# Kernel optimization log

Measured on AMD Instinct MI355X. Metric: run time of the kernel, lower is better.

## Reference

```python
import jax, jax.numpy as jnp
import numpy as np

N = 100000      # nodes
E = 1600000     # directed edges (before self loops)
F_IN = 128      # n_features
H = 100         # hidden width of every GCNConv / fc1
N_HIDDEN = 8    # conv2..conv9


def setup_inputs() -> dict:
    key = jax.random.key(0)
    ks = jax.random.split(key, 12)
    s = 0.05
    x = jax.random.normal(ks[0], (N, F_IN), jnp.float32)
    edge_index = jax.random.randint(ks[1], (2, E), 0, N, dtype=jnp.int64)
    labels = (jax.random.uniform(ks[2], (N, 1)) < 0.1).astype(jnp.float32)
    W1 = jax.random.normal(ks[3], (F_IN, H), jnp.float32) * s
    b1 = jnp.zeros((H,), jnp.float32)
    Wh = jax.random.normal(ks[4], (N_HIDDEN, H, H), jnp.float32) * s
    bh = jnp.zeros((N_HIDDEN, H), jnp.float32)
    fc1_W = jax.random.normal(ks[5], (H, H), jnp.float32) * s
    fc1_b = jnp.zeros((H,), jnp.float32)
    fc2_W = jax.random.normal(ks[6], (H, 1), jnp.float32) * s
    fc2_b = jnp.zeros((1,), jnp.float32)
    return {"x": x, "edge_index": edge_index, "labels": labels,
            "W1": W1, "b1": b1, "Wh": Wh, "bh": bh,
            "fc1_W": fc1_W, "fc1_b": fc1_b, "fc2_W": fc2_W, "fc2_b": fc2_b}


def _gcn_conv(h, W, b, src, dst, norm):
    # linear transform, then degree-normalized scatter aggregation (PyG GCNConv)
    h = h @ W                                   # [N, H]
    msg = h[src] * norm[:, None]                # [E2, H] gather + scale
    agg = jax.ops.segment_sum(msg, dst, num_segments=N)  # scatter-add to [N, H]
    return agg + b


def reference(x, edge_index, labels, W1, b1, Wh, bh, fc1_W, fc1_b, fc2_W, fc2_b):
    # GCN normalization with self loops: norm_e = deg^-1/2[src] * deg^-1/2[dst]
    loops = jnp.arange(N, dtype=edge_index.dtype)
    src = jnp.concatenate([edge_index[0], loops])
    dst = jnp.concatenate([edge_index[1], loops])
    deg = jax.ops.segment_sum(jnp.ones_like(dst, jnp.float32), dst, num_segments=N)
    dinv = jax.lax.rsqrt(deg)                   # deg >= 1 due to self loops
    norm = dinv[src] * dinv[dst]

    # NOTE: source uses x.relu() (out-of-place, discarded) -> no nonlinearity;
    # dropout is identity in eval mode. Faithful reproduction below.
    h = _gcn_conv(x, W1, b1, src, dst, norm)
    for i in range(N_HIDDEN):
        h = _gcn_conv(h, Wh[i], bh[i], src, dst, norm)

    h = h @ fc1_W + fc1_b
    logits = h @ fc2_W + fc2_b
    p = jax.nn.sigmoid(logits)                  # [N, 1]

    # generate_weights: upweight positives by neg/pos ratio
    pos = labels.sum()
    w = ((jnp.float32(N) - pos) / pos) * labels + 1.0

    pc = jnp.clip(p, 1e-7, 1.0 - 1e-7)
    bce = -(labels * jnp.log(pc) + (1.0 - labels) * jnp.log(1.0 - pc))
    loss = jnp.mean(w * bce)
    return loss, p
```

## Files before the change

### kernel.cpp

```cpp
#include <hip/hip_runtime.h>
#include <hip/hip_fp16.h>
#include <math.h>

#define HW 100
#define FIN 128
#define NBLK 256
#define TPB 1024
#define CHUNK 392
#define PBLK 512
#define BCAP 64
#define ELDS 7424
#define M17 0x1FFFFu
#define NPADH 100352

typedef int iv4 __attribute__((ext_vector_type(4)));

__device__ __forceinline__ float ld_dev(const float* p) {
    return __hip_atomic_load(p, __ATOMIC_RELAXED, __HIP_MEMORY_SCOPE_AGENT);
}
__device__ __forceinline__ unsigned ld_devu(const unsigned* p) {
    return __hip_atomic_load(p, __ATOMIC_RELAXED, __HIP_MEMORY_SCOPE_AGENT);
}
__device__ __forceinline__ void st_devu(unsigned* p, unsigned v) {
    __hip_atomic_store(p, v, __ATOMIC_RELAXED, __HIP_MEMORY_SCOPE_AGENT);
}
__device__ __forceinline__ void st_devh(__half* p, __half v) {
    __hip_atomic_store(reinterpret_cast<unsigned short*>(p),
                       *reinterpret_cast<unsigned short*>(&v),
                       __ATOMIC_RELAXED, __HIP_MEMORY_SCOPE_AGENT);
}

__global__ __launch_bounds__(256) void k_prep(const int* __restrict__ src,
                                              const int* __restrict__ dst, int E4,
                                              unsigned* __restrict__ buckets,
                                              int* __restrict__ cnt,
                                              float* __restrict__ accums,
                                              unsigned* __restrict__ posDone,
                                              unsigned* __restrict__ fin,
                                              unsigned* __restrict__ flags,
                                              const float* __restrict__ W1, const float* __restrict__ b1,
                                              const float* __restrict__ Wh, const float* __restrict__ bh,
                                              const float* __restrict__ fc1W, const float* __restrict__ fc1b,
                                              const float* __restrict__ fc2W, const float* __restrict__ fc2b,
                                              float* __restrict__ wstar, float* __restrict__ gammas) {
    int tid = threadIdx.x;
    if (blockIdx.x == 0) {
        __shared__ float v[HW], vn[HW];
        for (int i = tid; i < NBLK * 16; i += 256) flags[i] = 0u;
        if (tid < HW) v[tid] = fc2W[tid];
        __syncthreads();
        if (tid < HW) { float a = 0.f; for (int c = 0; c < HW; ++c) a += fc1W[tid * HW + c] * v[c]; vn[tid] = a; }
        __syncthreads();
        if (tid < HW) v[tid] = vn[tid];
        __syncthreads();
        if (tid == 0) {
            float a = 0.f; for (int c = 0; c < HW; ++c) a += bh[7 * HW + c] * v[c];
            float b = 0.f; for (int c = 0; c < HW; ++c) b += fc1b[c] * fc2W[c];
            gammas[9] = a + b + fc2b[0];
        }
        __syncthreads();
        for (int i = 7; i >= 0; --i) {
            const float* M = Wh + (size_t)i * HW * HW;
            if (tid < HW) { float a = 0.f; for (int c = 0; c < HW; ++c) a += M[tid * HW + c] * v[c]; vn[tid] = a; }
            __syncthreads();
            if (tid < HW) v[tid] = vn[tid];
            __syncthreads();
            if (tid == 0) {
                const float* bb = (i >= 1) ? (bh + (size_t)(i - 1) * HW) : b1;
                float a = 0.f; for (int c = 0; c < HW; ++c) a += bb[c] * v[c];
                gammas[i + 1] = a;
            }
            __syncthreads();
        }
        if (tid < FIN) { float a = 0.f; for (int c = 0; c < HW; ++c) a += W1[tid * HW + c] * v[c]; wstar[tid] = a; }
        if (tid == 0) { accums[0] = 0.f; accums[1] = 0.f; *posDone = 0u; *fin = 0u; }
        return;
    }
    __shared__ int cur[NBLK];
    int pb = blockIdx.x - 1;
    if (tid < NBLK) cur[tid] = 0;
    __syncthreads();
    const iv4* d4 = reinterpret_cast<const iv4*>(dst);
    const iv4* s4 = reinterpret_cast<const iv4*>(src);
    int i = pb * 256 + tid;
    int stride = PBLK * 256;
    for (; i < E4; i += stride) {
        iv4 d = __builtin_nontemporal_load(d4 + i);
        iv4 s = __builtin_nontemporal_load(s4 + i);
        #pragma unroll
        for (int q = 0; q < 4; ++q) {
            unsigned dd = (unsigned)d[q];
            unsigned ss = (unsigned)s[q];
            unsigned c = (unsigned)(((unsigned long long)dd * 171634ull) >> 26);
            unsigned ldst = dd - c * 391u;
            int pos = atomicAdd(&cur[c], 1);
            if (pos < BCAP)
                buckets[((size_t)c * PBLK + pb) * BCAP + pos] = ss | (ldst << 17);
        }
    }
    __syncthreads();
    if (tid < NBLK) cnt[(size_t)pb * NBLK + tid] = cur[tid];
}

__global__ __launch_bounds__(TPB) void k_main(const float* __restrict__ x,
        const float* __restrict__ labels,
        const float* __restrict__ wstar, const float* __restrict__ gammas,
        const int* __restrict__ cntG, const unsigned* __restrict__ bucketsG,
        __half* __restrict__ ubase,
        float* __restrict__ accums, unsigned* __restrict__ flags,
        unsigned* __restrict__ posDone, unsigned* __restrict__ fin,
        float* __restrict__ outF, int N) {
    __shared__ alignas(16) float ws[FIN];
    __shared__ float gam[16];
    __shared__ int   cntL[PBLK], incl[PBLK];
    __shared__ int   degLi[CHUNK];
    __shared__ float dinvL[CHUNK], uownL[CHUNK], yownL[CHUNK], accL[CHUNK];
    __shared__ float red[TPB];
    __shared__ alignas(16) unsigned myE[ELDS];

    int tid = threadIdx.x;
    int b = blockIdx.x;
    int chunk = (N + NBLK - 1) / NBLK;
    int nlo = b * chunk; if (nlo > N) nlo = N;
    int nhi = nlo + chunk; if (nhi > N) nhi = N;
    int nn = nhi - nlo;

    if (tid < FIN) ws[tid] = wstar[tid];
    if (tid < 16) gam[tid] = gammas[tid];
    for (int r = tid; r < CHUNK; r += TPB) degLi[r] = 0;
    if (tid < PBLK) { int v = cntG[(size_t)tid * NBLK + b]; cntL[tid] = v; incl[tid] = v; }
    __syncthreads();
    for (int off = 1; off < PBLK; off <<= 1) {
        int v = (tid < PBLK && tid >= off) ? incl[tid - off] : 0;
        __syncthreads();
        if (tid < PBLK) incl[tid] += v;
        __syncthreads();
    }
    int ecnt = incl[PBLK - 1];
    if (ecnt > ELDS) ecnt = ELDS;

    const unsigned* col = bucketsG + (size_t)b * PBLK * BCAP;
    for (int idx = tid; idx < PBLK * BCAP; idx += TPB) {
        int p = idx >> 6, j = idx & (BCAP - 1);
        int c = cntL[p];
        if (j < c) {
            unsigned e = col[(size_t)p * BCAP + j];
            int o = incl[p] - c + j;
            if (o < ELDS) { myE[o] = e; atomicAdd(&degLi[e >> 17], 1); }
        }
    }
    __syncthreads();
    for (int r = tid; r < nn; r += TPB) dinvL[r] = rsqrtf((float)degLi[r] + 1.0f);
    __syncthreads();

    {
        int wid = tid >> 6, half = (tid >> 5) & 1, l32 = tid & 31;
        int pcnt = (nn + 1) >> 1;
        const float4* x4 = reinterpret_cast<const float4*>(x);
        for (int pb = wid; pb < pcnt; pb += 16) {
            int ln = pb * 2 + half;
            float dsum = 0.f;
            if (ln < nn) {
                float4 xv = x4[(size_t)(nlo + ln) * (FIN / 4) + l32];
                float4 wv = *reinterpret_cast<const float4*>(&ws[l32 * 4]);
                dsum = xv.x * wv.x + xv.y * wv.y + xv.z * wv.z + xv.w * wv.w;
            }
            #pragma unroll
            for (int off = 16; off; off >>= 1) dsum += __shfl_down(dsum, off, 32);
            if (l32 == 0 && ln < nn) {
                float u0 = dsum * dinvL[ln];
                uownL[ln] = u0;
                st_devh(&ubase[nlo + ln], __float2half(u0));
            }
        }
    }
    asm volatile("s_waitcnt vmcnt(0)" ::: "memory");
    {
        float s = 0.f;
        for (int ln = tid; ln < nn; ln += TPB) s += labels[nlo + ln];
        red[tid] = s; __syncthreads();
        for (int off = TPB / 2; off; off >>= 1) {
            if (tid < off) red[tid] += red[tid + off];
            __syncthreads();
        }
        if (tid == 0) {
            atomicAdd(&accums[0], red[0]);
            asm volatile("s_waitcnt vmcnt(0)" ::: "memory");
            __hip_atomic_fetch_add(posDone, 1u, __ATOMIC_RELAXED, __HIP_MEMORY_SCOPE_AGENT);
            st_devu(&flags[b * 16], 1u);
        }
    }

    for (int k = 1; k <= 9; ++k) {
        const __half* ubr = ubase + (size_t)(k - 1) * NPADH;
        __half* ubw = ubase + (size_t)k * NPADH;
        float gk = gam[k];
        for (int ln = tid; ln < nn; ln += TPB) accL[ln] = uownL[ln];
        if (tid < NBLK)
            while (ld_devu(&flags[tid * 16]) < (unsigned)k) __builtin_amdgcn_s_sleep(1);
        __syncthreads();
        int ecnt8 = ecnt & ~7;
        for (int e = tid * 8; e < ecnt8; e += TPB * 8) {
            uint4 pA = *reinterpret_cast<const uint4*>(&myE[e]);
            uint4 pB = *reinterpret_cast<const uint4*>(&myE[e + 4]);
            float f0 = __half2float(ubr[pA.x & M17]);
            float f1 = __half2float(ubr[pA.y & M17]);
            float f2 = __half2float(ubr[pA.z & M17]);
            float f3 = __half2float(ubr[pA.w & M17]);
            float f4 = __half2float(ubr[pB.x & M17]);
            float f5 = __half2float(ubr[pB.y & M17]);
            float f6 = __half2float(ubr[pB.z & M17]);
            float f7 = __half2float(ubr[pB.w & M17]);
            atomicAdd(&accL[pA.x >> 17], f0);
            atomicAdd(&accL[pA.y >> 17], f1);
            atomicAdd(&accL[pA.z >> 17], f2);
            atomicAdd(&accL[pA.w >> 17], f3);
            atomicAdd(&accL[pB.x >> 17], f4);
            atomicAdd(&accL[pB.y >> 17], f5);
            atomicAdd(&accL[pB.z >> 17], f6);
            atomicAdd(&accL[pB.w >> 17], f7);
        }
        for (int e = ecnt8 + tid; e < ecnt; e += TPB) {
            unsigned p = myE[e];
            atomicAdd(&accL[p >> 17], __half2float(ubr[p & M17]));
        }
        __syncthreads();
        for (int ln = tid; ln < nn; ln += TPB) {
            float di = dinvL[ln];
            float y = di * accL[ln] + gk;
            float nu = di * y;
            uownL[ln] = nu;
            if (k < 9) st_devh(&ubw[nlo + ln], __float2half(nu));
            else yownL[ln] = y;
        }
        if (k < 9) {
            asm volatile("s_waitcnt vmcnt(0)" ::: "memory");
            __syncthreads();
            if (tid == 0) st_devu(&flags[b * 16], (unsigned)(k + 1));
        }
    }
    __syncthreads();

    if (tid == 0)
        while (ld_devu(posDone) < NBLK) __builtin_amdgcn_s_sleep(2);
    __syncthreads();
    {
        float pos = ld_dev(&accums[0]);
        float wpos = ((float)N - pos) / pos;
        float acc = 0.f;
        for (int ln = tid; ln < nn; ln += TPB) {
            float y = yownL[ln];
            float pp = 1.f / (1.f + expf(-y));
            outF[1 + nlo + ln] = pp;
            float pc = fminf(fmaxf(pp, 1e-7f), 1.f - 1e-7f);
            float l = labels[nlo + ln];
            float w = wpos * l + 1.f;
            acc += w * (-(l * logf(pc) + (1.f - l) * logf(1.f - pc)));
        }
        red[tid] = acc; __syncthreads();
        for (int off = TPB / 2; off; off >>= 1) {
            if (tid < off) red[tid] += red[tid + off];
            __syncthreads();
        }
        if (tid == 0) {
            atomicAdd(&accums[1], red[0]);
            asm volatile("s_waitcnt vmcnt(0)" ::: "memory");
            unsigned old = __hip_atomic_fetch_add(fin, 1u, __ATOMIC_RELAXED, __HIP_MEMORY_SCOPE_AGENT);
            if (old == NBLK - 1u)
                outF[0] = ld_dev(&accums[1]) / (float)N;
        }
    }
}

extern "C" void kernel_launch(void* const* d_in, const int* in_sizes, int n_in,
                              void* d_out, int out_size, void* d_ws, size_t ws_size,
                              hipStream_t stream) {
    const float* x      = (const float*)d_in[0];
    const int*   edge   = (const int*)d_in[1];
    const float* labels = (const float*)d_in[2];
    const float* W1     = (const float*)d_in[3];
    const float* b1     = (const float*)d_in[4];
    const float* Wh     = (const float*)d_in[5];
    const float* bh     = (const float*)d_in[6];
    const float* fc1W   = (const float*)d_in[7];
    const float* fc1b   = (const float*)d_in[8];
    const float* fc2W   = (const float*)d_in[9];
    const float* fc2b   = (const float*)d_in[10];

    const int N = in_sizes[0] / FIN;
    const int E = in_sizes[1] / 2;
    const int* srcIdx = edge;
    const int* dstIdx = edge + E;

    size_t o = 0;
    auto carve = [&](size_t bytes) {
        void* p = (char*)d_ws + o;
        o += (bytes + 511) & ~(size_t)511;
        return p;
    };
    float*    accums  = (float*)   carve(4 * 4);
    unsigned* posDone = (unsigned*)carve(4);
    unsigned* fin     = (unsigned*)carve(4);
    unsigned* flags   = (unsigned*)carve((size_t)NBLK * 16 * 4);
    float*    wstar   = (float*)   carve(FIN * 4);
    float*    gammas  = (float*)   carve(16 * 4);
    __half*   ubase   = (__half*)  carve((size_t)NPADH * 10 * 2);
    int*      cnt     = (int*)     carve((size_t)PBLK * NBLK * 4);
    unsigned* buckets = (unsigned*)carve((size_t)NBLK * PBLK * BCAP * 4);
    (void)ws_size; (void)n_in; (void)out_size;

    k_prep<<<PBLK + 1, 256, 0, stream>>>(srcIdx, dstIdx, E / 4, buckets, cnt,
                                         accums, posDone, fin, flags,
                                         W1, b1, Wh, bh, fc1W, fc1b, fc2W, fc2b,
                                         wstar, gammas);

    float* outF = (float*)d_out;
    int Nv = N;
    void* args[] = {(void*)&x, (void*)&labels, (void*)&wstar, (void*)&gammas,
                    (void*)&cnt, (void*)&buckets, (void*)&ubase,
                    (void*)&accums, (void*)&flags, (void*)&posDone, (void*)&fin,
                    (void*)&outF, (void*)&Nv};
    hipError_t err = hipLaunchCooperativeKernel((const void*)k_main, dim3(NBLK), dim3(TPB),
                                                args, 0, stream);
    (void)err;
}
```

Baseline: 197.4 us.

## Replace fixed-capacity edge buckets with compact per-slice counting-sort layout

The edge binning pass now gives each prep block a contiguous slice of 3200 edges. It counts destination buckets first, prefix-scans them, and writes the edges compactly with per-bucket offsets, instead of into fixed 64-slot padded buckets. The main kernel reads each producer's segment through the offsets, one thread per producer, with a serial inner loop. This removes the padded bucket memory and the capacity overflow drop, at the cost of a second pass over dst, an extra offsets array, and less coalesced per-thread serial reads in the main kernel. It hardcodes E=1.6M as 500 slices of 3200 edges.

```diff
diff --git a/kernel.cpp b/kernel.cpp
--- a/kernel.cpp
+++ b/kernel.cpp
@@ -7,8 +7,9 @@
 #define NBLK 256
 #define TPB 1024
 #define CHUNK 392
-#define PBLK 512
-#define BCAP 64
+#define PBLK 500
+#define SLICE 3200
+#define SL4 800
 #define ELDS 7424
 #define M17 0x1FFFFu
 #define NPADH 100352
@@ -31,9 +32,9 @@
 }
 
 __global__ __launch_bounds__(256) void k_prep(const int* __restrict__ src,
-                                              const int* __restrict__ dst, int E4,
+                                              const int* __restrict__ dst,
                                               unsigned* __restrict__ buckets,
-                                              int* __restrict__ cnt,
+                                              int* __restrict__ cntG, int* __restrict__ ofsG,
                                               float* __restrict__ accums,
                                               unsigned* __restrict__ posDone,
                                               unsigned* __restrict__ fin,
@@ -76,43 +77,68 @@
         if (tid == 0) { accums[0] = 0.f; accums[1] = 0.f; *posDone = 0u; *fin = 0u; }
         return;
     }
-    __shared__ int cur[NBLK];
-    int pb = blockIdx.x - 1;
+    __shared__ int cur[NBLK], wr[NBLK];
+    int p = blockIdx.x - 1;
     if (tid < NBLK) cur[tid] = 0;
     __syncthreads();
-    const iv4* d4 = reinterpret_cast<const iv4*>(dst);
-    const iv4* s4 = reinterpret_cast<const iv4*>(src);
-    int i = pb * 256 + tid;
-    int stride = PBLK * 256;
-    for (; i < E4; i += stride) {
-        iv4 d = __builtin_nontemporal_load(d4 + i);
-        iv4 s = __builtin_nontemporal_load(s4 + i);
+    const iv4* d4 = reinterpret_cast<const iv4*>(dst) + (size_t)p * SL4;
+    const iv4* s4 = reinterpret_cast<const iv4*>(src) + (size_t)p * SL4;
+    for (int i = tid; i < SL4; i += 256) {
+        iv4 d = d4[i];
+        #pragma unroll
+        for (int q = 0; q < 4; ++q) {
+            unsigned dd = (unsigned)d[q];
+            unsigned c = (unsigned)(((unsigned long long)dd * 171634ull) >> 26);
+            atomicAdd(&cur[c], 1);
+        }
+    }
+    __syncthreads();
+    {
+        __shared__ int sc[NBLK];
+        if (tid < NBLK) sc[tid] = cur[tid];
+        __syncthreads();
+        for (int off = 1; off < NBLK; off <<= 1) {
+            int v = (tid < NBLK && tid >= off) ? sc[tid - off] : 0;
+            __syncthreads();
+            if (tid < NBLK) sc[tid] += v;
+            __syncthreads();
+        }
+        if (tid < NBLK) {
+            int o = sc[tid] - cur[tid];
+            wr[tid] = o;
+            cntG[(size_t)p * NBLK + tid] = cur[tid];
+            ofsG[(size_t)p * NBLK + tid] = o;
+        }
+    }
+    __syncthreads();
+    unsigned* out = buckets + (size_t)p * SLICE;
+    for (int i = tid; i < SL4; i += 256) {
+        iv4 d = d4[i];
+        iv4 s = s4[i];
         #pragma unroll
         for (int q = 0; q < 4; ++q) {
             unsigned dd = (unsigned)d[q];
             unsigned ss = (unsigned)s[q];
             unsigned c = (unsigned)(((unsigned long long)dd * 171634ull) >> 26);
             unsigned ldst = dd - c * 391u;
-            int pos = atomicAdd(&cur[c], 1);
-            if (pos < BCAP)
-                buckets[((size_t)c * PBLK + pb) * BCAP + pos] = ss | (ldst << 17);
-        }
-    }
-    __syncthreads();
-    if (tid < NBLK) cnt[(size_t)pb * NBLK + tid] = cur[tid];
+            int pos = atomicAdd(&wr[c], 1);
+            out[pos] = ss | (ldst << 17);
+        }
+    }
 }
 
 __global__ __launch_bounds__(TPB) void k_main(const float* __restrict__ x,
         const float* __restrict__ labels,
         const float* __restrict__ wstar, const float* __restrict__ gammas,
-        const int* __restrict__ cntG, const unsigned* __restrict__ bucketsG,
+        const int* __restrict__ cntG, const int* __restrict__ ofsG,
+        const unsigned* __restrict__ bucketsG,
         __half* __restrict__ ubase,
         float* __restrict__ accums, unsigned* __restrict__ flags,
         unsigned* __restrict__ posDone, unsigned* __restrict__ fin,
         float* __restrict__ outF, int N) {
     __shared__ alignas(16) float ws[FIN];
     __shared__ float gam[16];
-    __shared__ int   cntL[PBLK], incl[PBLK];
+    __shared__ int   cntL[512], incl[512], ofsL[512];
     __shared__ int   degLi[CHUNK];
     __shared__ float dinvL[CHUNK], uownL[CHUNK], yownL[CHUNK], accL[CHUNK];
     __shared__ float red[TPB];
@@ -128,25 +154,28 @@
     if (tid < FIN) ws[tid] = wstar[tid];
     if (tid < 16) gam[tid] = gammas[tid];
     for (int r = tid; r < CHUNK; r += TPB) degLi[r] = 0;
-    if (tid < PBLK) { int v = cntG[(size_t)tid * NBLK + b]; cntL[tid] = v; incl[tid] = v; }
-    __syncthreads();
-    for (int off = 1; off < PBLK; off <<= 1) {
-        int v = (tid < PBLK && tid >= off) ? incl[tid - off] : 0;
-        __syncthreads();
-        if (tid < PBLK) incl[tid] += v;
-        __syncthreads();
-    }
-    int ecnt = incl[PBLK - 1];
+    if (tid < 512) {
+        int v = (tid < PBLK) ? cntG[(size_t)tid * NBLK + b] : 0;
+        cntL[tid] = v; incl[tid] = v;
+        ofsL[tid] = (tid < PBLK) ? ofsG[(size_t)tid * NBLK + b] : 0;
+    }
+    __syncthreads();
+    for (int off = 1; off < 512; off <<= 1) {
+        int v = (tid < 512 && tid >= off) ? incl[tid - off] : 0;
+        __syncthreads();
+        if (tid < 512) incl[tid] += v;
+        __syncthreads();
+    }
+    int ecnt = incl[511];
     if (ecnt > ELDS) ecnt = ELDS;
 
-    const unsigned* col = bucketsG + (size_t)b * PBLK * BCAP;
-    for (int idx = tid; idx < PBLK * BCAP; idx += TPB) {
-        int p = idx >> 6, j = idx & (BCAP - 1);
+    for (int p = tid; p < PBLK; p += TPB) {
         int c = cntL[p];
-        if (j < c) {
-            unsigned e = col[(size_t)p * BCAP + j];
-            int o = incl[p] - c + j;
-            if (o < ELDS) { myE[o] = e; atomicAdd(&degLi[e >> 17], 1); }
+        int g = p * SLICE + ofsL[p];
+        int lb = incl[p] - c;
+        for (int j = 0; j < c; ++j) {
+            unsigned e = bucketsG[g + j];
+            if (lb + j < ELDS) { myE[lb + j] = e; atomicAdd(&degLi[e >> 17], 1); }
         }
     }
     __syncthreads();
@@ -306,10 +335,11 @@
     float*    gammas  = (float*)   carve(16 * 4);
     __half*   ubase   = (__half*)  carve((size_t)NPADH * 10 * 2);
     int*      cnt     = (int*)     carve((size_t)PBLK * NBLK * 4);
-    unsigned* buckets = (unsigned*)carve((size_t)NBLK * PBLK * BCAP * 4);
+    int*      ofs     = (int*)     carve((size_t)PBLK * NBLK * 4);
+    unsigned* buckets = (unsigned*)carve((size_t)PBLK * SLICE * 4);
     (void)ws_size; (void)n_in; (void)out_size;
 
-    k_prep<<<PBLK + 1, 256, 0, stream>>>(srcIdx, dstIdx, E / 4, buckets, cnt,
+    k_prep<<<PBLK + 1, 256, 0, stream>>>(srcIdx, dstIdx, buckets, cnt, ofs,
                                          accums, posDone, fin, flags,
                                          W1, b1, Wh, bh, fc1W, fc1b, fc2W, fc2b,
                                          wstar, gammas);
@@ -317,7 +347,7 @@
     float* outF = (float*)d_out;
     int Nv = N;
     void* args[] = {(void*)&x, (void*)&labels, (void*)&wstar, (void*)&gammas,
-                    (void*)&cnt, (void*)&buckets, (void*)&ubase,
+                    (void*)&cnt, (void*)&ofs, (void*)&buckets, (void*)&ubase,
                     (void*)&accums, (void*)&flags, (void*)&posDone, (void*)&fin,
                     (void*)&outF, (void*)&Nv};
     hipError_t err = hipLaunchCooperativeKernel((const void*)k_main, dim3(NBLK), dim3(TPB),
```

Result: faster. 186.0 us (-5.8%).
